# Optimization experiments

Hardware: AMD Instinct MI355X
Metric: run time of the kernel (lower is better)

The kernel has to match this reference:

```python
import jax, jax.numpy as jnp
import numpy as np

EPS = 1e-8
H, DH = 4, 8
HID = H * DH  # 32
FF = 20       # 4 * dim
C = 5         # channels per degree


def snorm(x):
    # grad-safe L2 norm over last axis
    return jnp.sqrt(jnp.sum(x * x, axis=-1) + 1e-12)


def _ln(v, gamma, beta):
    mu = v.mean(-1, keepdims=True)
    sd = v.std(-1, keepdims=True) + EPS
    return (v - mu) / sd * gamma + beta


def norm_se3(x0, x1, g, b):
    # equivariant norm: transform per-channel invariant norms, keep orientation (phase)
    n0 = jnp.abs(x0)
    y0 = jnp.sign(x0) * jax.nn.gelu(_ln(n0, g[0], b[0]))
    n1 = snorm(x1)                                        # (b,n,c)
    y1 = x1 / n1[..., None] * jax.nn.gelu(_ln(n1, g[1], b[1]))[..., None]
    return y0, y1


def attention(x0, x1, coors, adjm, Wq, Mk, Mv, R1, rb1, R2, rb2, Wo0, Wo1):
    b, n, c = x0.shape
    rel = coors[:, None, :, :] - coors[:, :, None, :]     # (b,i,j,3): x_j - x_i
    dist = jnp.sqrt(jnp.sum(rel * rel, -1, keepdims=True) + 1e-12)
    u = rel / dist                                        # unit directions
    # radial net -> per-edge kernel coefficients for each degree-pair/basis (k and v)
    phi = jax.nn.relu(dist @ R1 + rb1) @ R2 + rb2         # (b,i,j,12*HID)
    (k00, k10, k01, kI, kU, kX, v00, v10, v01, vI, vU, vX) = jnp.split(phi, 12, -1)

    def edge_feats(M, p00, p10, p01, pI, pU, pX):
        y00 = jnp.einsum('bjc,ch->bjh', x0, M[0])
        y10 = jnp.einsum('bjcm,ch->bjhm', x1, M[1])
        y01 = jnp.einsum('bjc,ch->bjh', x0, M[2])
        yI = jnp.einsum('bjcm,ch->bjhm', x1, M[3])
        yU = jnp.einsum('bjcm,ch->bjhm', x1, M[4])
        yX = jnp.einsum('bjcm,ch->bjhm', x1, M[5])
        # degree-0 messages: (0->0) scalar and (1->0) vector.dot(u) paths
        e0 = p00 * y00[:, None] + p10 * jnp.einsum('bjhm,bijm->bijh', y10, u)
        un = u[:, :, :, None, :]                          # (b,i,j,1,3)
        # degree-1 messages: closed-form equivariant bases u*s, I, u(u.v), u x v
        e1 = (p01[..., None] * y01[:, None, :, :, None] * un
              + pI[..., None] * yI[:, None]
              + pU[..., None] * jnp.einsum('bjhm,bijm->bijh', yU, u)[..., None] * un
              + pX[..., None] * jnp.cross(un, yX[:, None]))
        return e0, e1

    k0, k1 = edge_feats(Mk, k00, k10, k01, kI, kU, kX)
    v0, v1 = edge_feats(Mv, v00, v10, v01, vI, vU, vX)

    q0 = jnp.einsum('bic,ch->bih', x0, Wq[0]).reshape(b, n, H, DH)
    q1 = jnp.einsum('bicm,ch->bihm', x1, Wq[1]).reshape(b, n, H, DH, 3)
    logits = (jnp.einsum('bihd,bijhd->bhij', q0, k0.reshape(b, n, n, H, DH))
              + jnp.einsum('bihdm,bijhdm->bhij', q1, k1.reshape(b, n, n, H, DH, 3)))
    logits = logits / jnp.asarray(DH, x0.dtype) ** 0.5
    logits = jnp.where(adjm[:, None], logits, -1e9)       # sparse-neighbor mask
    attn = jax.nn.softmax(logits, axis=-1)
    o0 = jnp.einsum('bhij,bijhd->bihd', attn, v0.reshape(b, n, n, H, DH)).reshape(b, n, HID)
    o1 = jnp.einsum('bhij,bijhdm->bihdm', attn, v1.reshape(b, n, n, H, DH, 3)).reshape(b, n, HID, 3)
    return o0 @ Wo0, jnp.einsum('bnhm,hc->bncm', o1, Wo1)


def feedforward(x0, x1, Wf1, Wf2, gs, bs):
    h0 = jax.nn.gelu(jnp.einsum('bnc,cf->bnf', x0, Wf1[0]))
    h1 = jnp.einsum('bncm,cf->bnfm', x1, Wf1[1])
    h1 = h1 * jax.nn.sigmoid(snorm(h1) * gs + bs)[..., None]   # norm-gated nonlin (equivariant)
    return jnp.einsum('bnf,fc->bnc', h0, Wf2[0]), jnp.einsum('bnfm,fc->bncm', h1, Wf2[1])


def _forward(feats, coors, adj_mat, Wq, Mk, Mv, R1, rb1, R2, rb2, Wo0, Wo1, gnA, bnA, gnF, bnF, Wf1, Wf2, gs, bs, Wh1, bh1, Wh2, bh2):
    b, n, _ = feats.shape
    a = adj_mat.astype(jnp.float32)
    # num_adj_degrees=2: attend over 1-hop OR 2-hop neighbors (plus self)
    adjm = adj_mat | ((a @ a) > 0) | jnp.eye(n, dtype=bool)
    x0 = feats
    x1 = jnp.zeros(feats.shape + (3,), feats.dtype)       # input fiber has only degree-0
    x0n, x1n = norm_se3(x0, x1, gnA, bnA)
    d0, d1 = attention(x0n, x1n, coors, adjm, Wq, Mk, Mv, R1, rb1, R2, rb2, Wo0, Wo1)
    x0, x1 = x0 + d0, x1 + d1
    x0n, x1n = norm_se3(x0, x1, gnF, bnF)
    f0, f1 = feedforward(x0n, x1n, Wf1, Wf2, gs, bs)
    x0, x1 = x0 + f0, x1 + f1
    pooled = x0.mean(axis=1)                              # mean pool type-0 features
    h = jax.nn.relu(pooled @ Wh1 + bh1)
    out = h @ Wh2 + bh2                                   # (b, 9)
    return out.reshape(-1, 3, 3)


def setup_inputs():
    key = jax.random.key(0)
    ks = jax.random.split(key, 16)
    B, N = 2, 256
    g = lambda i, shape, s: jax.random.normal(ks[i], shape, jnp.float32) * s
    feats = g(0, (B, N, C), 1.0)
    coors = g(1, (B, N, 3), 3.0)
    r = jax.random.uniform(ks[2], (B, N, N))
    adj = r < 0.03
    adj = (adj | jnp.swapaxes(adj, 1, 2)) & ~jnp.eye(N, dtype=bool)
    s5, sh, sf, s128 = C ** -0.5, HID ** -0.5, FF ** -0.5, 128 ** -0.5
    return dict(
        feats=feats, coors=coors, adj_mat=adj,
        Wq=g(3, (2, C, HID), s5), Mk=g(4, (6, C, HID), s5), Mv=g(5, (6, C, HID), s5),
        R1=g(6, (1, 32), 1.0), rb1=jnp.zeros(32), R2=g(7, (32, 12 * HID), 32 ** -0.5), rb2=jnp.zeros(12 * HID),
        Wo0=g(8, (HID, C), sh), Wo1=g(9, (HID, C), sh),
        gnA=jnp.ones((2, C)), bnA=jnp.zeros((2, C)), gnF=jnp.ones((2, C)), bnF=jnp.zeros((2, C)),
        Wf1=g(10, (2, C, FF), s5), Wf2=g(11, (2, FF, C), sf), gs=jnp.ones(FF), bs=jnp.zeros(FF),
        Wh1=g(12, (C, 128), s5), bh1=jnp.zeros(128), Wh2=g(13, (128, 9), s128), bh2=jnp.zeros(9))


def reference(feats, coors, adj_mat, Wq, Mk, Mv, R1, rb1, R2, rb2, Wo0, Wo1, gnA, bnA, gnF, bnF, Wf1, Wf2, gs, bs, Wh1, bh1, Wh2, bh2):
    return _forward(feats, coors, adj_mat, Wq, Mk, Mv, R1, rb1, R2, rb2, Wo0, Wo1, gnA, bnA, gnF, bnF, Wf1, Wf2, gs, bs, Wh1, bh1, Wh2, bh2)
```

## Files before the change

kernel.cpp:

```cpp
#include <hip/hip_runtime.h>
#include <math.h>

#define BB 2
#define NN 256
#define CC 5
#define HIDD 32


__device__ __forceinline__ float gelu_tanh(float x) {
    float x3 = x * x * x;
    return 0.5f * x * (1.0f + tanhf(0.7978845608028654f * (x + 0.044715f * x3)));
}
__device__ __forceinline__ float sgnf(float x) {
    return (x > 0.f) ? 1.f : ((x < 0.f) ? -1.f : 0.f);
}

#define TROW 9
#define TSZ (33 * TROW)

__global__ __launch_bounds__(256) void prep(
    const int* __restrict__ adj,
    const float* __restrict__ feats,
    const float* __restrict__ Wq0, const float* __restrict__ Mk0, const float* __restrict__ Mv0,
    const float* __restrict__ gnA0, const float* __restrict__ bnA0,
    const float* __restrict__ R1, const float* __restrict__ rb1,
    const float* __restrict__ R2, const float* __restrict__ rb2,
    unsigned long long* __restrict__ bits,
    float* __restrict__ q0, float* __restrict__ yk, float* __restrict__ yv,
    float* __restrict__ table,
    float* __restrict__ tsg)
{
    int bid = blockIdx.x;
    int tid = threadIdx.x;

    if (bid < 128) {
        int lane = tid & 63, wave = tid >> 6;
        int row = bid * 4 + wave;
#pragma unroll
        for (int k = 0; k < 4; k++) {
            int v = adj[(size_t)row * NN + k * 64 + lane];
            unsigned long long m = __ballot(v != 0);
            if (lane == 0) bits[row * 4 + k] = m;
        }
    } else if (bid < 192) {
        int node = (bid - 128) * 8 + (tid >> 5);
        int hd = tid & 31;
        const float* f = feats + node * CC;
        float n0[CC], x0n[CC];
        float mu = 0.f;
#pragma unroll
        for (int c = 0; c < CC; c++) { n0[c] = fabsf(f[c]); mu += n0[c]; }
        mu *= (1.0f / CC);
        float var = 0.f;
#pragma unroll
        for (int c = 0; c < CC; c++) { float d = n0[c] - mu; var += d * d; }
        var *= (1.0f / CC);
        float sd = sqrtf(var) + 1e-8f;
#pragma unroll
        for (int c = 0; c < CC; c++) {
            float ln = (n0[c] - mu) / sd * gnA0[c] + bnA0[c];
            x0n[c] = sgnf(f[c]) * gelu_tanh(ln);
        }
        float q = 0.f, k = 0.f, v = 0.f;
#pragma unroll
        for (int c = 0; c < CC; c++) {
            q = fmaf(x0n[c], Wq0[c * HIDD + hd], q);
            k = fmaf(x0n[c], Mk0[c * HIDD + hd], k);
            v = fmaf(x0n[c], Mv0[c * HIDD + hd], v);
        }
        q0[node * HIDD + hd] = q;
        yk[node * HIDD + hd] = k;
        yv[node * HIDD + hd] = v;
    } else {
        __shared__ float sR1[32], srb1[32], tt[32], ts[32], reps[33];
        if (tid < 32) { sR1[tid] = R1[tid]; srb1[tid] = rb1[tid]; }
        __syncthreads();
        if (tid < 32) {
            float r = sR1[tid];
            tt[tid] = (r != 0.f) ? (-srb1[tid] / r) : -3.0e38f;
        }
        __syncthreads();
        if (tid < 32) {
            float t = tt[tid];
            int rank = 0;
            for (int k = 0; k < 32; k++) {
                float tk = tt[k];
                rank += (tk < t) || (tk == t && k < tid);
            }
            ts[rank] = t;
        }
        __syncthreads();
        if (tid < 33) {
            float rep;
            if (tid == 0) rep = ts[0] - 1.0f;
            else if (tid == 32) rep = ts[31] + 1.0f;
            else rep = 0.5f * (ts[tid - 1] + ts[tid]);
            reps[tid] = rep;
            if (tid < 32) tsg[tid] = ts[tid];
        }
        __syncthreads();
        for (int idx = tid; idx < 33 * 32; idx += 256) {
            int p = idx >> 5, hd = idx & 31;
            float rep = reps[p];
            float A = 0.f, Bv = 0.f, Cv = 0.f, Dv = 0.f;
            for (int w = 0; w < 32; w++) {
                float r = sR1[w], bb = srb1[w];
                if (fmaf(r, rep, bb) > 0.f) {
                    float rk = R2[w * 384 + hd];
                    float rv = R2[w * 384 + 192 + hd];
                    A = fmaf(r, rk, A); Bv = fmaf(bb, rk, Bv);
                    Cv = fmaf(r, rv, Cv); Dv = fmaf(bb, rv, Dv);
                }
            }
            Bv += rb2[hd];
            Dv += rb2[192 + hd];
            table[0 * 33 * 36 + p * 36 + hd] = A;
            table[1 * 33 * 36 + p * 36 + hd] = Bv;
            table[2 * 33 * 36 + p * 36 + hd] = Cv;
            table[3 * 33 * 36 + p * 36 + hd] = Dv;
        }
    }
}

__global__ __launch_bounds__(256) void edge_attn(
    const float* __restrict__ coors,
    const float* __restrict__ q0g, const float* __restrict__ ykg, const float* __restrict__ yvg,
    const unsigned long long* __restrict__ bits,
    const float* __restrict__ feats,
    const float* __restrict__ Wo0,
    const float* __restrict__ gnF0, const float* __restrict__ bnF0,
    const float* __restrict__ Wf10,
    const float* __restrict__ Wf20,
    const float* __restrict__ table, const float* __restrict__ tsg,
    float* __restrict__ xfin)
{
    int node = blockIdx.x;
    int b = node >> 8, i = node & 255;
    int tid = threadIdx.x;
    int j = tid;
    int lane = tid & 63, wave = tid >> 6;

    __shared__ float4 sT[4 * TSZ];
    __shared__ float sts[32], q0s[32];
    __shared__ float Wo0t[5][32];
    __shared__ unsigned long long sbits[4];
    __shared__ float wredm[4][4], wreds[4][4], hm[4], hs[4];
    __shared__ float ew[4][5], x0as[5], xfs[5], h0s[20];

    {
        const float4* tg = (const float4*)table;
        for (int idx = tid; idx < 4 * TSZ; idx += 256) sT[idx] = tg[idx];
    }
    if (tid < 32) { sts[tid] = tsg[tid]; q0s[tid] = q0g[node * 32 + tid]; }
    if (tid < 160) Wo0t[tid / 32][tid % 32] = Wo0[(tid % 32) * 5 + tid / 32];
    if (tid < 4) sbits[tid] = bits[node * 4 + tid];
    __syncthreads();

    float dx = coors[(b * NN + j) * 3 + 0] - coors[(b * NN + i) * 3 + 0];
    float dy = coors[(b * NN + j) * 3 + 1] - coors[(b * NN + i) * 3 + 1];
    float dz = coors[(b * NN + j) * 3 + 2] - coors[(b * NN + i) * 3 + 2];
    float dist = sqrtf(dx * dx + dy * dy + dz * dz + 1e-12f);

    int p = 0;
#pragma unroll
    for (int k = 0; k < 32; k++) p += (sts[k] < dist) ? 1 : 0;

    const float4* Ap = sT + 0 * TSZ + p * TROW;
    const float4* Bp = sT + 1 * TSZ + p * TROW;
    const float4* Cp = sT + 2 * TSZ + p * TROW;
    const float4* Dp = sT + 3 * TSZ + p * TROW;
    const float4* ykp = (const float4*)(ykg + (size_t)(b * NN + j) * 32);
    const float4* yvp = (const float4*)(yvg + (size_t)(b * NN + j) * 32);
    const float4* q04 = (const float4*)q0s;

    float lg[4] = {0.f, 0.f, 0.f, 0.f};
#pragma unroll
    for (int q = 0; q < 8; q++) {
        float4 a = Ap[q], bb = Bp[q], y = ykp[q], qq = q04[q];
        int h = q >> 1;
        lg[h] = fmaf(fmaf(dist, a.x, bb.x) * qq.x, y.x, lg[h]);
        lg[h] = fmaf(fmaf(dist, a.y, bb.y) * qq.y, y.y, lg[h]);
        lg[h] = fmaf(fmaf(dist, a.z, bb.z) * qq.z, y.z, lg[h]);
        lg[h] = fmaf(fmaf(dist, a.w, bb.w) * qq.w, y.w, lg[h]);
    }

    {
        const unsigned long long* myb = bits + (size_t)(b * NN + j) * 4;
        bool direct = (sbits[j >> 6] >> (j & 63)) & 1ull;
        unsigned long long shr = (sbits[0] & myb[0]) | (sbits[1] & myb[1]) |
                                 (sbits[2] & myb[2]) | (sbits[3] & myb[3]);
        bool ok = direct || (shr != 0ull) || (i == j);
        const float invs = 0.35355339059327379f;
#pragma unroll
        for (int h = 0; h < 4; h++) lg[h] = ok ? lg[h] * invs : -1e9f;
    }

    float attn[4];
#pragma unroll
    for (int h = 0; h < 4; h++) {
        float v = lg[h];
        for (int off = 32; off; off >>= 1) v = fmaxf(v, __shfl_xor(v, off, 64));
        if (lane == 0) wredm[h][wave] = v;
    }
    __syncthreads();
    if (tid < 4) hm[tid] = fmaxf(fmaxf(wredm[tid][0], wredm[tid][1]), fmaxf(wredm[tid][2], wredm[tid][3]));
    __syncthreads();
#pragma unroll
    for (int h = 0; h < 4; h++) lg[h] = expf(lg[h] - hm[h]);
#pragma unroll
    for (int h = 0; h < 4; h++) {
        float v = lg[h];
        for (int off = 32; off; off >>= 1) v += __shfl_xor(v, off, 64);
        if (lane == 0) wreds[h][wave] = v;
    }
    __syncthreads();
    if (tid < 4) hs[tid] = wreds[tid][0] + wreds[tid][1] + wreds[tid][2] + wreds[tid][3];
    __syncthreads();
#pragma unroll
    for (int h = 0; h < 4; h++) attn[h] = lg[h] / hs[h];

    float e[5] = {0.f, 0.f, 0.f, 0.f, 0.f};
#pragma unroll
    for (int q = 0; q < 8; q++) {
        float4 c4 = Cp[q], d4 = Dp[q], y = yvp[q];
        float at = attn[q >> 1];
        float4 pv;
        pv.x = at * fmaf(dist, c4.x, d4.x) * y.x;
        pv.y = at * fmaf(dist, c4.y, d4.y) * y.y;
        pv.z = at * fmaf(dist, c4.z, d4.z) * y.z;
        pv.w = at * fmaf(dist, c4.w, d4.w) * y.w;
#pragma unroll
        for (int c = 0; c < 5; c++) {
            float4 w4 = ((const float4*)Wo0t[c])[q];
            e[c] = fmaf(pv.x, w4.x, fmaf(pv.y, w4.y, fmaf(pv.z, w4.z, fmaf(pv.w, w4.w, e[c]))));
        }
    }
    for (int off = 32; off; off >>= 1)
#pragma unroll
        for (int c = 0; c < 5; c++) e[c] += __shfl_xor(e[c], off, 64);
    if (lane == 0)
#pragma unroll
        for (int c = 0; c < 5; c++) ew[wave][c] = e[c];
    __syncthreads();

    if (tid < 5) {
        float d0 = ew[0][tid] + ew[1][tid] + ew[2][tid] + ew[3][tid];
        x0as[tid] = feats[node * 5 + tid] + d0;
    }
    __syncthreads();
    if (tid < 5) {
        float x0a[5], n0[5];
        float mu = 0.f;
#pragma unroll
        for (int c = 0; c < 5; c++) { x0a[c] = x0as[c]; n0[c] = fabsf(x0a[c]); mu += n0[c]; }
        mu *= 0.2f;
        float var = 0.f;
#pragma unroll
        for (int c = 0; c < 5; c++) { float d = n0[c] - mu; var += d * d; }
        var *= 0.2f;
        float sd = sqrtf(var) + 1e-8f;
        float ln = (n0[tid] - mu) / sd * gnF0[tid] + bnF0[tid];
        xfs[tid] = sgnf(x0a[tid]) * gelu_tanh(ln);
    }
    __syncthreads();
    if (tid < 20) {
        float s = 0.f;
#pragma unroll
        for (int c = 0; c < 5; c++) s = fmaf(xfs[c], Wf10[c * 20 + tid], s);
        h0s[tid] = gelu_tanh(s);
    }
    __syncthreads();
    if (tid < 5) {
        float f0 = 0.f;
        for (int f = 0; f < 20; f++) f0 = fmaf(h0s[f], Wf20[f * 5 + tid], f0);
        xfin[node * 5 + tid] = x0as[tid] + f0;
    }
}

__global__ __launch_bounds__(256) void head_mlp(const float* __restrict__ xfin,
                         const float* __restrict__ Wh1, const float* __restrict__ bh1,
                         const float* __restrict__ Wh2, const float* __restrict__ bh2,
                         float* __restrict__ out) {
    __shared__ float part[2][5][25];
    __shared__ float pooled[10];
    __shared__ float hdn[2][128];
    int tid = threadIdx.x;
    if (tid < 250) {
        int b = tid / 125, r = tid % 125, c = r / 25, grp = r % 25;
        float s = 0.f;
        for (int i = grp; i < NN; i += 25) s += xfin[(b * NN + i) * 5 + c];
        part[b][c][grp] = s;
    }
    __syncthreads();
    if (tid < 10) {
        int b = tid / 5, c = tid % 5;
        float s = 0.f;
        for (int g = 0; g < 25; g++) s += part[b][c][g];
        pooled[tid] = s * (1.0f / NN);
    }
    __syncthreads();
    {
        int b = tid >> 7, k = tid & 127;
        float s = bh1[k];
#pragma unroll
        for (int c = 0; c < 5; c++) s = fmaf(pooled[b * 5 + c], Wh1[c * 128 + k], s);
        hdn[b][k] = fmaxf(s, 0.f);
    }
    __syncthreads();
    if (tid < 18) {
        int b = tid / 9, o = tid % 9;
        float s = bh2[o];
        for (int k = 0; k < 128; k++) s = fmaf(hdn[b][k], Wh2[k * 9 + o], s);
        out[b * 9 + o] = s;
    }
}

extern "C" void kernel_launch(void* const* d_in, const int* in_sizes, int n_in,
                              void* d_out, int out_size, void* d_ws, size_t ws_size,
                              hipStream_t stream) {
    const float* feats = (const float*)d_in[0];
    const float* coors = (const float*)d_in[1];
    const int*   adj   = (const int*)d_in[2];
    const float* Wq    = (const float*)d_in[3];
    const float* Mk    = (const float*)d_in[4];
    const float* Mv    = (const float*)d_in[5];
    const float* R1    = (const float*)d_in[6];
    const float* rb1   = (const float*)d_in[7];
    const float* R2    = (const float*)d_in[8];
    const float* rb2   = (const float*)d_in[9];
    const float* Wo0   = (const float*)d_in[10];
    const float* gnA   = (const float*)d_in[12];
    const float* bnA   = (const float*)d_in[13];
    const float* gnF   = (const float*)d_in[14];
    const float* bnF   = (const float*)d_in[15];
    const float* Wf1   = (const float*)d_in[16];
    const float* Wf2   = (const float*)d_in[17];
    const float* Wh1   = (const float*)d_in[20];
    const float* bh1   = (const float*)d_in[21];
    const float* Wh2   = (const float*)d_in[22];
    const float* bh2   = (const float*)d_in[23];
    float* out = (float*)d_out;

    float* q0    = (float*)d_ws;
    float* yk    = q0 + 512 * 32;
    float* yv    = yk + 512 * 32;
    float* xfin  = yv + 512 * 32;
    float* tsg   = xfin + 512 * 8;
    unsigned long long* bits = (unsigned long long*)(tsg + 32);
    float* table = (float*)(bits + 512 * 4);

    hipLaunchKernelGGL(prep, dim3(193), dim3(256), 0, stream,
                       adj, feats, Wq, Mk, Mv, gnA, bnA, R1, rb1, R2, rb2,
                       bits, q0, yk, yv, table, tsg);
    hipLaunchKernelGGL(edge_attn, dim3(512), dim3(256), 0, stream,
                       coors, q0, yk, yv, bits, feats, Wo0, gnF, bnF, Wf1, Wf2,
                       table, tsg, xfin);
    hipLaunchKernelGGL(head_mlp, dim3(1), dim3(256), 0, stream,
                       xfin, Wh1, bh1, Wh2, bh2, out);
}
```

Baseline: 135.6 us.

## Fuse prep into attention kernel, recomputing per-block tables and projections

Removes the separate prep kernel. Each attention block now rebuilds the radial piecewise-linear table in shared memory, computes q/k/v projections inline per neighbor, and builds the two-hop adjacency mask by listing direct neighbors and gathering adj rows instead of using bitmasks. This drops one launch and the global workspace round trip. In exchange it duplicates the table build and the projection work across all 512 blocks, adds extra syncs, and raises register pressure (ykr/yvr arrays).

```diff
diff --git a/kernel.cpp b/kernel.cpp
--- a/kernel.cpp
+++ b/kernel.cpp
@@ -18,120 +18,18 @@
 #define TROW 9
 #define TSZ (33 * TROW)
 
-__global__ __launch_bounds__(256) void prep(
+__global__ __launch_bounds__(256) void fused_attn(
+    const float* __restrict__ coors,
     const int* __restrict__ adj,
     const float* __restrict__ feats,
     const float* __restrict__ Wq0, const float* __restrict__ Mk0, const float* __restrict__ Mv0,
     const float* __restrict__ gnA0, const float* __restrict__ bnA0,
     const float* __restrict__ R1, const float* __restrict__ rb1,
     const float* __restrict__ R2, const float* __restrict__ rb2,
-    unsigned long long* __restrict__ bits,
-    float* __restrict__ q0, float* __restrict__ yk, float* __restrict__ yv,
-    float* __restrict__ table,
-    float* __restrict__ tsg)
-{
-    int bid = blockIdx.x;
-    int tid = threadIdx.x;
-
-    if (bid < 128) {
-        int lane = tid & 63, wave = tid >> 6;
-        int row = bid * 4 + wave;
-#pragma unroll
-        for (int k = 0; k < 4; k++) {
-            int v = adj[(size_t)row * NN + k * 64 + lane];
-            unsigned long long m = __ballot(v != 0);
-            if (lane == 0) bits[row * 4 + k] = m;
-        }
-    } else if (bid < 192) {
-        int node = (bid - 128) * 8 + (tid >> 5);
-        int hd = tid & 31;
-        const float* f = feats + node * CC;
-        float n0[CC], x0n[CC];
-        float mu = 0.f;
-#pragma unroll
-        for (int c = 0; c < CC; c++) { n0[c] = fabsf(f[c]); mu += n0[c]; }
-        mu *= (1.0f / CC);
-        float var = 0.f;
-#pragma unroll
-        for (int c = 0; c < CC; c++) { float d = n0[c] - mu; var += d * d; }
-        var *= (1.0f / CC);
-        float sd = sqrtf(var) + 1e-8f;
-#pragma unroll
-        for (int c = 0; c < CC; c++) {
-            float ln = (n0[c] - mu) / sd * gnA0[c] + bnA0[c];
-            x0n[c] = sgnf(f[c]) * gelu_tanh(ln);
-        }
-        float q = 0.f, k = 0.f, v = 0.f;
-#pragma unroll
-        for (int c = 0; c < CC; c++) {
-            q = fmaf(x0n[c], Wq0[c * HIDD + hd], q);
-            k = fmaf(x0n[c], Mk0[c * HIDD + hd], k);
-            v = fmaf(x0n[c], Mv0[c * HIDD + hd], v);
-        }
-        q0[node * HIDD + hd] = q;
-        yk[node * HIDD + hd] = k;
-        yv[node * HIDD + hd] = v;
-    } else {
-        __shared__ float sR1[32], srb1[32], tt[32], ts[32], reps[33];
-        if (tid < 32) { sR1[tid] = R1[tid]; srb1[tid] = rb1[tid]; }
-        __syncthreads();
-        if (tid < 32) {
-            float r = sR1[tid];
-            tt[tid] = (r != 0.f) ? (-srb1[tid] / r) : -3.0e38f;
-        }
-        __syncthreads();
-        if (tid < 32) {
-            float t = tt[tid];
-            int rank = 0;
-            for (int k = 0; k < 32; k++) {
-                float tk = tt[k];
-                rank += (tk < t) || (tk == t && k < tid);
-            }
-            ts[rank] = t;
-        }
-        __syncthreads();
-        if (tid < 33) {
-            float rep;
-            if (tid == 0) rep = ts[0] - 1.0f;
-            else if (tid == 32) rep = ts[31] + 1.0f;
-            else rep = 0.5f * (ts[tid - 1] + ts[tid]);
-            reps[tid] = rep;
-            if (tid < 32) tsg[tid] = ts[tid];
-        }
-        __syncthreads();
-        for (int idx = tid; idx < 33 * 32; idx += 256) {
-            int p = idx >> 5, hd = idx & 31;
-            float rep = reps[p];
-            float A = 0.f, Bv = 0.f, Cv = 0.f, Dv = 0.f;
-            for (int w = 0; w < 32; w++) {
-                float r = sR1[w], bb = srb1[w];
-                if (fmaf(r, rep, bb) > 0.f) {
-                    float rk = R2[w * 384 + hd];
-                    float rv = R2[w * 384 + 192 + hd];
-                    A = fmaf(r, rk, A); Bv = fmaf(bb, rk, Bv);
-                    Cv = fmaf(r, rv, Cv); Dv = fmaf(bb, rv, Dv);
-                }
-            }
-            Bv += rb2[hd];
-            Dv += rb2[192 + hd];
-            table[0 * 33 * 36 + p * 36 + hd] = A;
-            table[1 * 33 * 36 + p * 36 + hd] = Bv;
-            table[2 * 33 * 36 + p * 36 + hd] = Cv;
-            table[3 * 33 * 36 + p * 36 + hd] = Dv;
-        }
-    }
-}
-
-__global__ __launch_bounds__(256) void edge_attn(
-    const float* __restrict__ coors,
-    const float* __restrict__ q0g, const float* __restrict__ ykg, const float* __restrict__ yvg,
-    const unsigned long long* __restrict__ bits,
-    const float* __restrict__ feats,
     const float* __restrict__ Wo0,
     const float* __restrict__ gnF0, const float* __restrict__ bnF0,
     const float* __restrict__ Wf10,
     const float* __restrict__ Wf20,
-    const float* __restrict__ table, const float* __restrict__ tsg,
     float* __restrict__ xfin)
 {
     int node = blockIdx.x;
@@ -141,26 +39,137 @@
     int lane = tid & 63, wave = tid >> 6;
 
     __shared__ float4 sT[4 * TSZ];
-    __shared__ float sts[32], q0s[32];
+    __shared__ float R2k[32][32];
+    __shared__ float R2v[32][32];
+    __shared__ float sR1[32], srb1[32], tt[32], sts[32];
+    __shared__ float q0s[32];
     __shared__ float Wo0t[5][32];
-    __shared__ unsigned long long sbits[4];
+    __shared__ int nlist[NN];
+    __shared__ int ncnt;
     __shared__ float wredm[4][4], wreds[4][4], hm[4], hs[4];
     __shared__ float ew[4][5], x0as[5], xfs[5], h0s[20];
 
-    {
-        const float4* tg = (const float4*)table;
-        for (int idx = tid; idx < 4 * TSZ; idx += 256) sT[idx] = tg[idx];
-    }
-    if (tid < 32) { sts[tid] = tsg[tid]; q0s[tid] = q0g[node * 32 + tid]; }
+    int av = adj[(size_t)(b * NN + i) * NN + j];
+
+    for (int idx = tid; idx < 1024; idx += 256) {
+        int w = idx >> 5, hd = idx & 31;
+        R2k[w][hd] = R2[w * 384 + hd];
+        R2v[w][hd] = R2[w * 384 + 192 + hd];
+    }
+    if (tid < 32) { sR1[tid] = R1[tid]; srb1[tid] = rb1[tid]; }
     if (tid < 160) Wo0t[tid / 32][tid % 32] = Wo0[(tid % 32) * 5 + tid / 32];
-    if (tid < 4) sbits[tid] = bits[node * 4 + tid];
-    __syncthreads();
+    if (tid == 0) ncnt = 0;
 
     float dx = coors[(b * NN + j) * 3 + 0] - coors[(b * NN + i) * 3 + 0];
     float dy = coors[(b * NN + j) * 3 + 1] - coors[(b * NN + i) * 3 + 1];
     float dz = coors[(b * NN + j) * 3 + 2] - coors[(b * NN + i) * 3 + 2];
     float dist = sqrtf(dx * dx + dy * dy + dz * dz + 1e-12f);
 
+    float x0n[CC];
+    {
+        const float* f = feats + (size_t)(b * NN + j) * CC;
+        float fv[CC], n0[CC];
+        float mu = 0.f;
+#pragma unroll
+        for (int c = 0; c < CC; c++) { fv[c] = f[c]; n0[c] = fabsf(fv[c]); mu += n0[c]; }
+        mu *= (1.0f / CC);
+        float var = 0.f;
+#pragma unroll
+        for (int c = 0; c < CC; c++) { float d = n0[c] - mu; var += d * d; }
+        var *= (1.0f / CC);
+        float sd = sqrtf(var) + 1e-8f;
+#pragma unroll
+        for (int c = 0; c < CC; c++) {
+            float ln = (n0[c] - mu) / sd * gnA0[c] + bnA0[c];
+            x0n[c] = sgnf(fv[c]) * gelu_tanh(ln);
+        }
+    }
+
+    __syncthreads();
+
+    if (tid < 32) {
+        float r = sR1[tid];
+        tt[tid] = (r != 0.f) ? (-srb1[tid] / r) : -3.0e38f;
+    }
+    if (av) { int p = atomicAdd(&ncnt, 1); nlist[p] = j; }
+    if (tid < 32) {
+        const float* f = feats + (size_t)(b * NN + i) * CC;
+        float fv[CC], n0[CC], xi[CC];
+        float mu = 0.f;
+#pragma unroll
+        for (int c = 0; c < CC; c++) { fv[c] = f[c]; n0[c] = fabsf(fv[c]); mu += n0[c]; }
+        mu *= (1.0f / CC);
+        float var = 0.f;
+#pragma unroll
+        for (int c = 0; c < CC; c++) { float d = n0[c] - mu; var += d * d; }
+        var *= (1.0f / CC);
+        float sd = sqrtf(var) + 1e-8f;
+#pragma unroll
+        for (int c = 0; c < CC; c++) {
+            float ln = (n0[c] - mu) / sd * gnA0[c] + bnA0[c];
+            xi[c] = sgnf(fv[c]) * gelu_tanh(ln);
+        }
+        float q = 0.f;
+#pragma unroll
+        for (int c = 0; c < CC; c++) q = fmaf(xi[c], Wq0[c * HIDD + tid], q);
+        q0s[tid] = q;
+    }
+    float ykr[32];
+#pragma unroll
+    for (int hd = 0; hd < 32; hd++) ykr[hd] = 0.f;
+#pragma unroll
+    for (int c = 0; c < CC; c++) {
+        float xc = x0n[c];
+#pragma unroll
+        for (int hd = 0; hd < 32; hd++)
+            ykr[hd] = fmaf(xc, Mk0[c * HIDD + hd], ykr[hd]);
+    }
+    __syncthreads();
+
+    if (tid < 32) {
+        float t = tt[tid];
+        int rank = 0;
+        for (int k = 0; k < 32; k++) {
+            float tk = tt[k];
+            rank += (tk < t) || (tk == t && k < tid);
+        }
+        sts[rank] = t;
+    }
+    int okacc = (av != 0) || (i == j);
+    {
+        int cnt = ncnt;
+        for (int t = 0; t < cnt; t++) {
+            int m = nlist[t];
+            okacc |= adj[(size_t)(b * NN + m) * NN + j];
+        }
+    }
+    __syncthreads();
+
+    for (int idx = tid; idx < 33 * 32; idx += 256) {
+        int p = idx >> 5, hd = idx & 31;
+        float rep = (p == 0) ? (sts[0] - 1.0f)
+                  : (p == 32) ? (sts[31] + 1.0f)
+                  : 0.5f * (sts[p - 1] + sts[p]);
+        float A = 0.f, Bv = 0.f, Cv = 0.f, Dv = 0.f;
+        for (int w = 0; w < 32; w++) {
+            float r = sR1[w], bb = srb1[w];
+            if (fmaf(r, rep, bb) > 0.f) {
+                float rk = R2k[w][hd];
+                float rv = R2v[w][hd];
+                A = fmaf(r, rk, A); Bv = fmaf(bb, rk, Bv);
+                Cv = fmaf(r, rv, Cv); Dv = fmaf(bb, rv, Dv);
+            }
+        }
+        Bv += rb2[hd];
+        Dv += rb2[192 + hd];
+        float* tf = (float*)sT;
+        tf[(0 * TSZ + p * TROW) * 4 + hd] = A;
+        tf[(1 * TSZ + p * TROW) * 4 + hd] = Bv;
+        tf[(2 * TSZ + p * TROW) * 4 + hd] = Cv;
+        tf[(3 * TSZ + p * TROW) * 4 + hd] = Dv;
+    }
+    __syncthreads();
+
     int p = 0;
 #pragma unroll
     for (int k = 0; k < 32; k++) p += (sts[k] < dist) ? 1 : 0;
@@ -169,28 +178,21 @@
     const float4* Bp = sT + 1 * TSZ + p * TROW;
     const float4* Cp = sT + 2 * TSZ + p * TROW;
     const float4* Dp = sT + 3 * TSZ + p * TROW;
-    const float4* ykp = (const float4*)(ykg + (size_t)(b * NN + j) * 32);
-    const float4* yvp = (const float4*)(yvg + (size_t)(b * NN + j) * 32);
     const float4* q04 = (const float4*)q0s;
 
     float lg[4] = {0.f, 0.f, 0.f, 0.f};
 #pragma unroll
     for (int q = 0; q < 8; q++) {
-        float4 a = Ap[q], bb = Bp[q], y = ykp[q], qq = q04[q];
+        float4 a = Ap[q], bb = Bp[q], qq = q04[q];
         int h = q >> 1;
-        lg[h] = fmaf(fmaf(dist, a.x, bb.x) * qq.x, y.x, lg[h]);
-        lg[h] = fmaf(fmaf(dist, a.y, bb.y) * qq.y, y.y, lg[h]);
-        lg[h] = fmaf(fmaf(dist, a.z, bb.z) * qq.z, y.z, lg[h]);
-        lg[h] = fmaf(fmaf(dist, a.w, bb.w) * qq.w, y.w, lg[h]);
-    }
-
+        lg[h] = fmaf(fmaf(dist, a.x, bb.x) * qq.x, ykr[4 * q + 0], lg[h]);
+        lg[h] = fmaf(fmaf(dist, a.y, bb.y) * qq.y, ykr[4 * q + 1], lg[h]);
+        lg[h] = fmaf(fmaf(dist, a.z, bb.z) * qq.z, ykr[4 * q + 2], lg[h]);
+        lg[h] = fmaf(fmaf(dist, a.w, bb.w) * qq.w, ykr[4 * q + 3], lg[h]);
+    }
     {
-        const unsigned long long* myb = bits + (size_t)(b * NN + j) * 4;
-        bool direct = (sbits[j >> 6] >> (j & 63)) & 1ull;
-        unsigned long long shr = (sbits[0] & myb[0]) | (sbits[1] & myb[1]) |
-                                 (sbits[2] & myb[2]) | (sbits[3] & myb[3]);
-        bool ok = direct || (shr != 0ull) || (i == j);
         const float invs = 0.35355339059327379f;
+        bool ok = okacc != 0;
 #pragma unroll
         for (int h = 0; h < 4; h++) lg[h] = ok ? lg[h] * invs : -1e9f;
     }
@@ -219,16 +221,27 @@
 #pragma unroll
     for (int h = 0; h < 4; h++) attn[h] = lg[h] / hs[h];
 
+    float yvr[32];
+#pragma unroll
+    for (int hd = 0; hd < 32; hd++) yvr[hd] = 0.f;
+#pragma unroll
+    for (int c = 0; c < CC; c++) {
+        float xc = x0n[c];
+#pragma unroll
+        for (int hd = 0; hd < 32; hd++)
+            yvr[hd] = fmaf(xc, Mv0[c * HIDD + hd], yvr[hd]);
+    }
+
     float e[5] = {0.f, 0.f, 0.f, 0.f, 0.f};
 #pragma unroll
     for (int q = 0; q < 8; q++) {
-        float4 c4 = Cp[q], d4 = Dp[q], y = yvp[q];
+        float4 c4 = Cp[q], d4 = Dp[q];
         float at = attn[q >> 1];
         float4 pv;
-        pv.x = at * fmaf(dist, c4.x, d4.x) * y.x;
-        pv.y = at * fmaf(dist, c4.y, d4.y) * y.y;
-        pv.z = at * fmaf(dist, c4.z, d4.z) * y.z;
-        pv.w = at * fmaf(dist, c4.w, d4.w) * y.w;
+        pv.x = at * fmaf(dist, c4.x, d4.x) * yvr[4 * q + 0];
+        pv.y = at * fmaf(dist, c4.y, d4.y) * yvr[4 * q + 1];
+        pv.z = at * fmaf(dist, c4.z, d4.z) * yvr[4 * q + 2];
+        pv.w = at * fmaf(dist, c4.w, d4.w) * yvr[4 * q + 3];
 #pragma unroll
         for (int c = 0; c < 5; c++) {
             float4 w4 = ((const float4*)Wo0t[c])[q];
@@ -341,20 +354,11 @@
     const float* bh2   = (const float*)d_in[23];
     float* out = (float*)d_out;
 
-    float* q0    = (float*)d_ws;
-    float* yk    = q0 + 512 * 32;
-    float* yv    = yk + 512 * 32;
-    float* xfin  = yv + 512 * 32;
-    float* tsg   = xfin + 512 * 8;
-    unsigned long long* bits = (unsigned long long*)(tsg + 32);
-    float* table = (float*)(bits + 512 * 4);
-
-    hipLaunchKernelGGL(prep, dim3(193), dim3(256), 0, stream,
-                       adj, feats, Wq, Mk, Mv, gnA, bnA, R1, rb1, R2, rb2,
-                       bits, q0, yk, yv, table, tsg);
-    hipLaunchKernelGGL(edge_attn, dim3(512), dim3(256), 0, stream,
-                       coors, q0, yk, yv, bits, feats, Wo0, gnF, bnF, Wf1, Wf2,
-                       table, tsg, xfin);
+    float* xfin = (float*)d_ws;
+
+    hipLaunchKernelGGL(fused_attn, dim3(512), dim3(256), 0, stream,
+                       coors, adj, feats, Wq, Mk, Mv, gnA, bnA, R1, rb1, R2, rb2,
+                       Wo0, gnF, bnF, Wf1, Wf2, xfin);
     hipLaunchKernelGGL(head_mlp, dim3(1), dim3(256), 0, stream,
                        xfin, Wh1, bh1, Wh2, bh2, out);
 }
```

Measured after the change: 129.3 us. -4.7%, faster.
